# Kernel tuning notes

Measured on AMD Instinct MI355X. Metric: run time of the kernel, lower is better.

Reference implementation:

```python
import jax, jax.numpy as jnp
import numpy as np

X_BOUND = (-51.2, 51.2, 0.8)
Y_BOUND = (-51.2, 51.2, 0.8)
Z_BOUND = (-5.0, 3.0, 0.5)
DOWNSAMPLE = 8
NX = int(round((X_BOUND[1] - X_BOUND[0]) / X_BOUND[2]))  # 128
NY = int(round((Y_BOUND[1] - Y_BOUND[0]) / Y_BOUND[2]))  # 128
NZ = int(round((Z_BOUND[1] - Z_BOUND[0]) / Z_BOUND[2]))  # 16


def _frustum():
    # (4, N) homogeneous BEV voxel-center coordinates, N = NX*NY*NZ
    xs = X_BOUND[0] + jnp.arange(NX, dtype=jnp.float32) * X_BOUND[2]
    ys = Y_BOUND[0] + jnp.arange(NY, dtype=jnp.float32) * Y_BOUND[2]
    zs = Z_BOUND[0] + jnp.arange(NZ, dtype=jnp.float32) * Z_BOUND[2]
    pts = jnp.stack(jnp.meshgrid(xs, ys, zs, indexing='ij')).reshape(3, -1)
    return jnp.concatenate([pts, jnp.ones((1, pts.shape[1]), jnp.float32)], axis=0)


def _grid_sample_bilinear(feat, u, v):
    # feat: (B,C,H,W); u,v: (B,N) normalized coords in [-1,1], align_corners=True,
    # padding_mode='zeros'. Returns (B,C,N).
    B, C, H, W = feat.shape
    x = (u + 1.0) * 0.5 * (W - 1)
    y = (v + 1.0) * 0.5 * (H - 1)
    finite = jnp.isfinite(x) & jnp.isfinite(y)
    x = jnp.where(finite, x, -10.0)  # push non-finite coords fully out of range -> 0
    y = jnp.where(finite, y, -10.0)
    x0 = jnp.floor(x); y0 = jnp.floor(y)
    x1 = x0 + 1.0;     y1 = y0 + 1.0
    wx1 = x - x0; wx0 = 1.0 - wx1
    wy1 = y - y0; wy0 = 1.0 - wy1
    feat_flat = feat.reshape(B, C, H * W)

    def corner(xi, yi, w):
        valid = (xi >= 0) & (xi < W) & (yi >= 0) & (yi < H)
        xi_ = jnp.clip(xi, 0, W - 1).astype(jnp.int32)
        yi_ = jnp.clip(yi, 0, H - 1).astype(jnp.int32)
        idx = yi_ * W + xi_  # (B,N)
        vals = jax.vmap(lambda f, i: f[:, i])(feat_flat, idx)  # (B,C,N)
        return vals * (w * valid.astype(feat.dtype))[:, None, :]

    out = (corner(x0, y0, wx0 * wy0) + corner(x1, y0, wx1 * wy0)
           + corner(x0, y1, wx0 * wy1) + corner(x1, y1, wx1 * wy1))
    return jnp.where(jnp.isnan(out), 0.0, out)


def setup_inputs() -> dict:
    key = jax.random.key(0)
    k1, k2, k3, k4 = jax.random.split(key, 4)
    B, C, H, W = 2, 80, 32, 88
    return {
        'img_feats': jax.random.normal(k1, (B, C, H, W), jnp.float32),
        'intrin_mat': jax.random.normal(k2, (B, 1, 4, 4), jnp.float32),
        'extrin_mat': jax.random.normal(k3, (B, 1, 4, 4), jnp.float32),
        'bda_mat': jax.random.normal(k4, (B, 4, 4), jnp.float32),
    }


def reference(img_feats, intrin_mat, extrin_mat, bda_mat):
    B, C, H, W = img_feats.shape
    frustum = _frustum()  # (4, N)
    # intrinsic[..., :2, :] /= downsample_factor
    scale = jnp.array([1.0 / DOWNSAMPLE, 1.0 / DOWNSAMPLE, 1.0], jnp.float32)[:, None]
    intrinsic = intrin_mat[..., :3, :3] * scale          # (B,1,3,3)
    extrinsic = extrin_mat[..., :3, :]                   # (B,1,3,4)
    proj = intrinsic @ extrinsic                         # (B,1,3,4)
    points = jnp.einsum('bij,jn->bin', bda_mat, frustum) # (B,4,N)
    pixels = jnp.einsum('bcij,bjn->bcin', proj, points)  # (B,1,3,N)
    u = pixels[:, 0, 0, :] / pixels[:, 0, 2, :]          # (B,N)
    v = pixels[:, 0, 1, :] / pixels[:, 0, 2, :]
    u = u / W * 2.0 - 1.0
    v = v / H * 2.0 - 1.0
    bev = _grid_sample_bilinear(img_feats, u, v)         # (B,C,N)
    return bev.reshape(B, C, NX, NY, NZ)
```

## Files before the change

kernel.cpp:

```cpp
#include <hip/hip_runtime.h>
#include <hip/hip_bf16.h>

#define NXg 128
#define NYg 128
#define NZg 16
#define NPT (NXg * NYg * NZg)
#define Hh 32
#define Ww 88
#define Cc 80
#define HWc (Hh * Ww)
#define CSPLIT 4
#define CPB (Cc / CSPLIT)
#define NG (Cc / 4)

__global__ __launch_bounds__(256) void fvt_regroup(
    const float* __restrict__ feat, float* __restrict__ featG, int total)
{
    int t = blockIdx.x * 256 + threadIdx.x;
    if (t >= total) return;
    int cc = t & 3; int r = t >> 2;
    int p = r % HWc; r /= HWc;
    int g = r % NG;  int b = r / NG;
    featG[t] = feat[(((b * NG + g) * 4 + cc) * HWc) + p];
}

__global__ __launch_bounds__(256) void fvt_kernel(
    const float* __restrict__ featG,
    const float* __restrict__ intrin,
    const float* __restrict__ extrin,
    const float* __restrict__ bda,
    float* __restrict__ out)
{
    const int b  = blockIdx.y;
    const int cq = blockIdx.z;
    const int t  = blockIdx.x * blockDim.x + threadIdx.x;
    const int n0 = t << 2;
    if (n0 >= NPT) return;

    const float* In = intrin + b * 16;
    const float* Ex = extrin + b * 16;
    const float* Bd = bda    + b * 16;

    float K[3][3];
#pragma unroll
    for (int r = 0; r < 3; ++r)
#pragma unroll
        for (int c = 0; c < 3; ++c)
            K[r][c] = In[r * 4 + c] * (r == 2 ? 1.0f : 0.125f);

    float P[3][4];
#pragma unroll
    for (int r = 0; r < 3; ++r)
#pragma unroll
        for (int c = 0; c < 4; ++c)
            P[r][c] = K[r][0] * Ex[0 * 4 + c] + K[r][1] * Ex[1 * 4 + c] + K[r][2] * Ex[2 * 4 + c];

    float M[3][4];
#pragma unroll
    for (int r = 0; r < 3; ++r)
#pragma unroll
        for (int c = 0; c < 4; ++c)
            M[r][c] = P[r][0] * Bd[0 * 4 + c] + P[r][1] * Bd[1 * 4 + c]
                    + P[r][2] * Bd[2 * 4 + c] + P[r][3] * Bd[3 * 4 + c];

    const int iz0 = n0 & (NZg - 1);
    const int iy  = (n0 >> 4) & (NYg - 1);
    const int ix  = n0 >> 11;
    const float xf = -51.2f + (float)ix * 0.8f;
    const float yf = -51.2f + (float)iy * 0.8f;

    int   idxb[4][4];
    float wgt [4][4];
    bool  vj  [4];
    bool  anyv = false;

#pragma unroll
    for (int j = 0; j < 4; ++j) {
        const float zf = -5.0f + (float)(iz0 + j) * 0.5f;

        const float px = M[0][0] * xf + M[0][1] * yf + M[0][2] * zf + M[0][3];
        const float py = M[1][0] * xf + M[1][1] * yf + M[1][2] * zf + M[1][3];
        const float pz = M[2][0] * xf + M[2][1] * yf + M[2][2] * zf + M[2][3];

        float u = px / pz;
        float v = py / pz;
        u = u / (float)Ww * 2.0f - 1.0f;
        v = v / (float)Hh * 2.0f - 1.0f;

        float x = (u + 1.0f) * 0.5f * (float)(Ww - 1);
        float y = (v + 1.0f) * 0.5f * (float)(Hh - 1);
        const bool fin = __builtin_isfinite(x) && __builtin_isfinite(y);
        x = fin ? x : -10.0f;
        y = fin ? y : -10.0f;

        const float x0 = floorf(x);
        const float y0 = floorf(y);
        const float x1 = x0 + 1.0f;
        const float y1 = y0 + 1.0f;
        const float wx1 = x - x0, wx0 = 1.0f - wx1;
        const float wy1 = y - y0, wy0 = 1.0f - wy1;

        const float cx[4] = {x0, x1, x0, x1};
        const float cy[4] = {y0, y0, y1, y1};
        const float cw[4] = {wx0 * wy0, wx1 * wy0, wx0 * wy1, wx1 * wy1};
        float wsum = 0.0f;
#pragma unroll
        for (int k = 0; k < 4; ++k) {
            const bool valid = (cx[k] >= 0.0f) && (cx[k] < (float)Ww) &&
                               (cy[k] >= 0.0f) && (cy[k] < (float)Hh);
            const float xc = fminf(fmaxf(cx[k], 0.0f), (float)(Ww - 1));
            const float yc = fminf(fmaxf(cy[k], 0.0f), (float)(Hh - 1));
            idxb[j][k] = ((int)yc * Ww + (int)xc) << 2;
            wgt [j][k] = valid ? cw[k] : 0.0f;
            wsum += wgt[j][k];
        }
        vj[j] = wsum > 0.0f;
        anyv |= vj[j];
    }

    float* ob = out + ((size_t)b * Cc + cq * CPB) * (size_t)NPT + n0;

    if (!anyv) {
        const float4 z4 = make_float4(0.0f, 0.0f, 0.0f, 0.0f);
#pragma unroll
        for (int q = 0; q < CPB; ++q)
            *reinterpret_cast<float4*>(ob + (size_t)q * NPT) = z4;
        return;
    }

    const float* fb = featG + ((size_t)b * NG + cq * (CPB / 4)) * (size_t)(HWc * 4);

#pragma unroll 2
    for (int cg = 0; cg < CPB / 4; ++cg) {
        const float* fg = fb + (size_t)cg * (HWc * 4);
        float acc[4][4];
#pragma unroll
        for (int cc = 0; cc < 4; ++cc)
#pragma unroll
            for (int j = 0; j < 4; ++j) acc[cc][j] = 0.0f;

#pragma unroll
        for (int j = 0; j < 4; ++j) {
            if (vj[j]) {
#pragma unroll
                for (int k = 0; k < 4; ++k) {
                    const float4 f = *reinterpret_cast<const float4*>(fg + idxb[j][k]);
                    const float wk = wgt[j][k];
                    acc[0][j] = fmaf(wk, f.x, acc[0][j]);
                    acc[1][j] = fmaf(wk, f.y, acc[1][j]);
                    acc[2][j] = fmaf(wk, f.z, acc[2][j]);
                    acc[3][j] = fmaf(wk, f.w, acc[3][j]);
                }
            }
        }
#pragma unroll
        for (int cc = 0; cc < 4; ++cc) {
            *reinterpret_cast<float4*>(ob + (size_t)(cg * 4 + cc) * NPT) =
                make_float4(acc[cc][0], acc[cc][1], acc[cc][2], acc[cc][3]);
        }
    }
}

extern "C" void kernel_launch(void* const* d_in, const int* in_sizes, int n_in,
                              void* d_out, int out_size, void* d_ws, size_t ws_size,
                              hipStream_t stream) {
    const float* feat   = (const float*)d_in[0];
    const float* intrin = (const float*)d_in[1];
    const float* extrin = (const float*)d_in[2];
    const float* bda    = (const float*)d_in[3];
    float* out   = (float*)d_out;
    float* featG = (float*)d_ws;

    const int B = in_sizes[0] / (Cc * HWc);
    const int total = B * Cc * HWc;

    fvt_regroup<<<(total + 255) / 256, 256, 0, stream>>>(feat, featG, total);

    dim3 block(256);
    dim3 grid(NPT / 4 / 256, B, CSPLIT);
    fvt_kernel<<<grid, block, 0, stream>>>(featG, intrin, extrin, bda, out);
}
```

Before: 42.83 us.

## Store features as fp16 and fetch horizontal corner pairs in one load

The regroup kernel now converts the channel-grouped features to fp16, packing four channels per pixel into 8 bytes. The gather then reads two adjacent x pixels with one 16-byte load per row, halving loads per sample, with x clamped so the pair stays in range and weights remapped to the lo/hi slots. This reduces gather bandwidth and instruction count. The cost is fp16 rounding of the features, which may exceed tolerance, plus extra weight-selection arithmetic.

Result: faster. 41.05 us (-4.2%).

```diff
diff --git a/kernel.cpp b/kernel.cpp
--- a/kernel.cpp
+++ b/kernel.cpp
@@ -1,5 +1,6 @@
 #include <hip/hip_runtime.h>
 #include <hip/hip_bf16.h>
+#include <hip/hip_fp16.h>
 
 #define NXg 128
 #define NYg 128
@@ -13,19 +14,30 @@
 #define CPB (Cc / CSPLIT)
 #define NG (Cc / 4)
 
-__global__ __launch_bounds__(256) void fvt_regroup(
-    const float* __restrict__ feat, float* __restrict__ featG, int total)
+__global__ __launch_bounds__(256) void fvt_tohalf(
+    const float* __restrict__ feat, unsigned short* __restrict__ featH, int total)
 {
     int t = blockIdx.x * 256 + threadIdx.x;
     if (t >= total) return;
-    int cc = t & 3; int r = t >> 2;
-    int p = r % HWc; r /= HWc;
+    int p = t % HWc; int r = t / HWc;
     int g = r % NG;  int b = r / NG;
-    featG[t] = feat[(((b * NG + g) * 4 + cc) * HWc) + p];
+    const float* src = feat + ((size_t)(b * Cc + g * 4)) * HWc + p;
+    ushort4 px;
+    px.x = __half_as_ushort(__float2half(src[0 * HWc]));
+    px.y = __half_as_ushort(__float2half(src[1 * HWc]));
+    px.z = __half_as_ushort(__float2half(src[2 * HWc]));
+    px.w = __half_as_ushort(__float2half(src[3 * HWc]));
+    *reinterpret_cast<ushort4*>(featH + (size_t)t * 4) = px;
+}
+
+union U2F2 { unsigned u; __half2 h; };
+__device__ __forceinline__ float2 cvt2(unsigned u) {
+    U2F2 c; c.u = u;
+    return __half22float2(c.h);
 }
 
 __global__ __launch_bounds__(256) void fvt_kernel(
-    const float* __restrict__ featG,
+    const unsigned short* __restrict__ featH,
     const float* __restrict__ intrin,
     const float* __restrict__ extrin,
     const float* __restrict__ bda,
@@ -69,9 +81,10 @@
     const float xf = -51.2f + (float)ix * 0.8f;
     const float yf = -51.2f + (float)iy * 0.8f;
 
-    int   idxb[4][4];
-    float wgt [4][4];
-    bool  vj  [4];
+    int   off[4][2];
+    float wlo[4][2];
+    float whi[4][2];
+    bool  vj [4];
     bool  anyv = false;
 
 #pragma unroll
@@ -100,20 +113,33 @@
         const float wx1 = x - x0, wx0 = 1.0f - wx1;
         const float wy1 = y - y0, wy0 = 1.0f - wy1;
 
-        const float cx[4] = {x0, x1, x0, x1};
-        const float cy[4] = {y0, y0, y1, y1};
-        const float cw[4] = {wx0 * wy0, wx1 * wy0, wx0 * wy1, wx1 * wy1};
-        float wsum = 0.0f;
-#pragma unroll
-        for (int k = 0; k < 4; ++k) {
-            const bool valid = (cx[k] >= 0.0f) && (cx[k] < (float)Ww) &&
-                               (cy[k] >= 0.0f) && (cy[k] < (float)Hh);
-            const float xc = fminf(fmaxf(cx[k], 0.0f), (float)(Ww - 1));
-            const float yc = fminf(fmaxf(cy[k], 0.0f), (float)(Hh - 1));
-            idxb[j][k] = ((int)yc * Ww + (int)xc) << 2;
-            wgt [j][k] = valid ? cw[k] : 0.0f;
-            wsum += wgt[j][k];
-        }
+        const bool vx0 = (x0 >= 0.0f) && (x0 < (float)Ww);
+        const bool vx1 = (x1 >= 0.0f) && (x1 < (float)Ww);
+        const bool vy0 = (y0 >= 0.0f) && (y0 < (float)Hh);
+        const bool vy1 = (y1 >= 0.0f) && (y1 < (float)Hh);
+        const float w00 = (vx0 && vy0) ? wx0 * wy0 : 0.0f;
+        const float w10 = (vx1 && vy0) ? wx1 * wy0 : 0.0f;
+        const float w01 = (vx0 && vy1) ? wx0 * wy1 : 0.0f;
+        const float w11 = (vx1 && vy1) ? wx1 * wy1 : 0.0f;
+
+        const float xb  = fminf(fmaxf(x0, 0.0f), 86.0f);
+        const float y0c = fminf(fmaxf(y0, 0.0f), 31.0f);
+        const float y1c = fminf(fmaxf(y1, 0.0f), 31.0f);
+
+        const int xbi = (int)xb;
+        off[0 * 0 + j][0] = ((int)y0c * Ww + xbi) * 4;
+        off[j][1]         = ((int)y1c * Ww + xbi) * 4;
+
+        const float lo_is_x0 = (x0 == xb) ? 1.0f : 0.0f;
+        const float lo_is_x1 = (x1 == xb) ? 1.0f : 0.0f;
+        const float hi_is_x0 = (x0 == xb + 1.0f) ? 1.0f : 0.0f;
+        const float hi_is_x1 = (x1 == xb + 1.0f) ? 1.0f : 0.0f;
+        wlo[j][0] = lo_is_x0 * w00 + lo_is_x1 * w10;
+        whi[j][0] = hi_is_x0 * w00 + hi_is_x1 * w10;
+        wlo[j][1] = lo_is_x0 * w01 + lo_is_x1 * w11;
+        whi[j][1] = hi_is_x0 * w01 + hi_is_x1 * w11;
+
+        const float wsum = w00 + w10 + w01 + w11;
         vj[j] = wsum > 0.0f;
         anyv |= vj[j];
     }
@@ -128,11 +154,11 @@
         return;
     }
 
-    const float* fb = featG + ((size_t)b * NG + cq * (CPB / 4)) * (size_t)(HWc * 4);
+    const unsigned short* fb = featH + ((size_t)b * NG + cq * (CPB / 4)) * (size_t)(HWc * 4);
 
 #pragma unroll 2
     for (int cg = 0; cg < CPB / 4; ++cg) {
-        const float* fg = fb + (size_t)cg * (HWc * 4);
+        const unsigned short* fg = fb + (size_t)cg * (HWc * 4);
         float acc[4][4];
 #pragma unroll
         for (int cc = 0; cc < 4; ++cc)
@@ -143,13 +169,18 @@
         for (int j = 0; j < 4; ++j) {
             if (vj[j]) {
 #pragma unroll
-                for (int k = 0; k < 4; ++k) {
-                    const float4 f = *reinterpret_cast<const float4*>(fg + idxb[j][k]);
-                    const float wk = wgt[j][k];
-                    acc[0][j] = fmaf(wk, f.x, acc[0][j]);
-                    acc[1][j] = fmaf(wk, f.y, acc[1][j]);
-                    acc[2][j] = fmaf(wk, f.z, acc[2][j]);
-                    acc[3][j] = fmaf(wk, f.w, acc[3][j]);
+                for (int k = 0; k < 2; ++k) {
+                    const uint4 raw = *reinterpret_cast<const uint4*>(fg + off[j][k]);
+                    const float wl = wlo[j][k];
+                    const float wh = whi[j][k];
+                    const float2 lo01 = cvt2(raw.x);
+                    const float2 lo23 = cvt2(raw.y);
+                    const float2 hi01 = cvt2(raw.z);
+                    const float2 hi23 = cvt2(raw.w);
+                    acc[0][j] = fmaf(wl, lo01.x, fmaf(wh, hi01.x, acc[0][j]));
+                    acc[1][j] = fmaf(wl, lo01.y, fmaf(wh, hi01.y, acc[1][j]));
+                    acc[2][j] = fmaf(wl, lo23.x, fmaf(wh, hi23.x, acc[2][j]));
+                    acc[3][j] = fmaf(wl, lo23.y, fmaf(wh, hi23.y, acc[3][j]));
                 }
             }
         }
@@ -168,15 +199,15 @@
     const float* intrin = (const float*)d_in[1];
     const float* extrin = (const float*)d_in[2];
     const float* bda    = (const float*)d_in[3];
-    float* out   = (float*)d_out;
-    float* featG = (float*)d_ws;
+    float* out = (float*)d_out;
+    unsigned short* featH = (unsigned short*)d_ws;
 
     const int B = in_sizes[0] / (Cc * HWc);
-    const int total = B * Cc * HWc;
-
-    fvt_regroup<<<(total + 255) / 256, 256, 0, stream>>>(feat, featG, total);
+    const int total = B * NG * HWc;
+
+    fvt_tohalf<<<(total + 255) / 256, 256, 0, stream>>>(feat, featH, total);
 
     dim3 block(256);
     dim3 grid(NPT / 4 / 256, B, CSPLIT);
-    fvt_kernel<<<grid, block, 0, stream>>>(featG, intrin, extrin, bda, out);
-}
+    fvt_kernel<<<grid, block, 0, stream>>>(featH, intrin, extrin, bda, out);
+}
```
